# Optimization experiments

Hardware: AMD Instinct MI355X
Metric: run time of the kernel (lower is better)

Reference implementation:

```python
import jax, jax.numpy as jnp
import numpy as np

B, T, D, HS = 8, 2048, 1024, 64  # batch, seq, num_embd, head_size


def setup_inputs() -> dict:
    key = jax.random.key(0)
    kc, kq, kk, kv = jax.random.split(key, 4)
    return {
        "context": jax.random.normal(kc, (B, T, D), dtype=jnp.float32),
        "Wq": jax.random.normal(kq, (D, HS), dtype=jnp.float32) * (D ** -0.5),
        "Wk": jax.random.normal(kk, (D, HS), dtype=jnp.float32) * (D ** -0.5),
        "Wv": jax.random.normal(kv, (D, HS), dtype=jnp.float32) * (D ** -0.5),
    }


def reference(context, Wq, Wk, Wv):
    # context: [B, T, D]; projections: [B, T, HS]
    q = context @ Wq
    k = context @ Wk
    v = context @ Wv
    scale = k.shape[-1] ** -0.5
    # scores: [B, T, T], causal mask, stable softmax (dropout p=0 -> identity)
    wei = jnp.einsum("btd,bsd->bts", q, k) * scale
    t = wei.shape[-1]
    causal = jnp.tril(jnp.ones((t, t), dtype=bool))
    wei = jnp.where(causal, wei, -jnp.inf)
    wei = jax.nn.softmax(wei, axis=-1)
    return jnp.einsum("bts,bsh->bth", wei, v)
```

## Files before the change

kernel.cpp:

```cpp
#include <hip/hip_runtime.h>
#include <math.h>

#define BB 8
#define TT 2048
#define DD 1024
#define HSZ 64

typedef __bf16 bf16_t;
typedef bf16_t bf16x8 __attribute__((ext_vector_type(8)));
typedef bf16_t bf16x4 __attribute__((ext_vector_type(4)));
typedef float f32x4 __attribute__((ext_vector_type(4)));

#define MFMA16(A, B, C) __builtin_amdgcn_mfma_f32_16x16x32_bf16(A, B, C, 0, 0, 0)


__global__ __launch_bounds__(256) void wt_convert(
    const float* __restrict__ Wq, const float* __restrict__ Wk,
    const float* __restrict__ Wv, bf16_t* __restrict__ Wtf)
{
    int id = blockIdx.x * 256 + threadIdx.x;
    int j = id & 7;
    int lane = (id >> 3) & 63;
    int chunk = (id >> 9) & 31;
    int nt = id >> 14;
    int l16 = lane & 15, quad = lane >> 4;
    int k = chunk * 32 + quad * 8 + j;
    int col = nt * 16 + l16;
    int m = col >> 6, ncol = col & 63;
    const float* W = (m == 0) ? Wq : (m == 1) ? Wk : Wv;
    float scl = (m == 0) ? 0.18033688f : 1.0f;
    Wtf[id] = (bf16_t)(W[k * HSZ + ncol] * scl);
}

__global__ __launch_bounds__(256, 3) void qkv_proj(
    const float* __restrict__ ctx, const bf16_t* __restrict__ Wtf,
    bf16_t* __restrict__ Q, bf16_t* __restrict__ Kf, bf16_t* __restrict__ Vf)
{
    __shared__ __align__(16) char smem_raw[16 * 1032 * 2];
    bf16_t (*As)[1032] = (bf16_t (*)[1032])smem_raw;
    f32x4 (*red)[4][64] = (f32x4 (*)[4][64])smem_raw;

    const int tid = threadIdx.x;
    const int w = tid >> 6, lane = tid & 63;
    const int quad = lane >> 4, l16 = lane & 15;
    const size_t row0 = (size_t)blockIdx.x * 16;
    const int k0 = w * 256;

    {
        const float4* csrc = (const float4*)(ctx + row0 * DD);
        #pragma unroll
        for (int i = 0; i < 16; ++i) {
            float4 v = csrc[i * 256 + tid];
            bf16x4 bv;
            bv[0] = (bf16_t)v.x; bv[1] = (bf16_t)v.y;
            bv[2] = (bf16_t)v.z; bv[3] = (bf16_t)v.w;
            *(bf16x4*)&As[i][tid * 4] = bv;
        }
    }
    __syncthreads();

    f32x4 acc[12];
    #pragma unroll
    for (int i = 0; i < 12; ++i) acc[i] = (f32x4){0.f, 0.f, 0.f, 0.f};

    const bf16_t* wbase = Wtf + lane * 8;

    #pragma unroll
    for (int kc = 0; kc < 256; kc += 32) {
        const int chunk = (k0 + kc) >> 5;
        bf16x8 bfr[12];
        #pragma unroll
        for (int nt = 0; nt < 12; ++nt)
            bfr[nt] = *(const bf16x8*)(wbase + ((size_t)nt * 32 + chunk) * 512);
        bf16x8 af = *(const bf16x8*)&As[l16][k0 + kc + quad * 8];
        #pragma unroll
        for (int nt = 0; nt < 12; ++nt)
            acc[nt] = MFMA16(af, bfr[nt], acc[nt]);
    }
    __syncthreads();

    const int bb   = (int)(row0 >> 11);
    const int tloc = (int)(row0 & 2047);
    const int kt   = tloc >> 6;
    const int nn   = (tloc >> 4) & 3;

    #pragma unroll
    for (int r = 0; r < 3; ++r) {
        if (r) __syncthreads();
        #pragma unroll
        for (int i = 0; i < 4; ++i) red[w][i][lane] = acc[r * 4 + i];
        __syncthreads();

        f32x4 s = red[0][w][lane];
        s += red[1][w][lane];
        s += red[2][w][lane];
        s += red[3][w][lane];

        if (r == 0) {
            const int col = w * 16 + l16;
            #pragma unroll
            for (int reg = 0; reg < 4; ++reg)
                Q[(row0 + quad * 4 + reg) * HSZ + col] = (bf16_t)s[reg];
        } else if (r == 1) {
            const int ks = w >> 1;
            const int quadf = (w & 1) * 2 + (l16 >> 3);
            const int jj = l16 & 7;
            const size_t fb = ((((size_t)bb * 32 + kt) * 4 + nn) * 2 + ks) * 512;
            #pragma unroll
            for (int reg = 0; reg < 4; ++reg)
                Kf[fb + (quadf * 16 + quad * 4 + reg) * 8 + jj] = (bf16_t)s[reg];
        } else {
            const int t0 = tloc + quad * 4;
            const int ks = (t0 >> 5) & 1;
            const int quadf = (t0 >> 3) & 3;
            const int j0 = t0 & 7;
            const size_t fb = ((((size_t)bb * 32 + kt) * 2 + ks) * 4 + w) * 512;
            bf16x4 v;
            #pragma unroll
            for (int reg = 0; reg < 4; ++reg) v[reg] = (bf16_t)s[reg];
            *(bf16x4*)(Vf + fb + (quadf * 16 + l16) * 8 + j0) = v;
        }
    }
}

__device__ __forceinline__ void load_kfrags(
    const bf16_t* __restrict__ Kf, size_t bofs, int kt, int lane, bf16x8* kf)
{
    const bf16_t* kbase = Kf + ((bofs + (size_t)kt) * 8) * 512 + lane * 8;
    #pragma unroll
    for (int i = 0; i < 8; ++i)
        kf[i] = *(const bf16x8*)(kbase + i * 512);
}

__global__ __launch_bounds__(64, 3) void attn_kernel(
    const bf16_t* __restrict__ Q, const bf16_t* __restrict__ Kf,
    const bf16_t* __restrict__ Vf,
    float* __restrict__ Opart, float* __restrict__ Lpart)
{
    __shared__ bf16_t Ps[16][76];

    const int lane = threadIdx.x;
    const int quad = lane >> 4, l16 = lane & 15;

    const int z = blockIdx.x;
    const int b = z & 7, c = z >> 3;
    const int j = 127 - (c >> 2);
    const int seg = c & 3;
    const size_t base = (size_t)b * TT * HSZ;
    const size_t bofs = (size_t)b * 32;
    const int ntile = (j >> 2) + 1, jm = j & 3;

    const bf16_t* qp = Q + base + (size_t)(j * 16 + l16) * HSZ + quad * 8;
    bf16x8 qf0 = *(const bf16x8*)qp;
    bf16x8 qf1 = *(const bf16x8*)(qp + 32);

    bf16x8 onesf;
    {
        bf16_t e = (l16 == 0) ? (bf16_t)1.0f : (bf16_t)0.0f;
        #pragma unroll
        for (int i = 0; i < 8; ++i) onesf[i] = e;
    }

    f32x4 o[4];
    #pragma unroll
    for (int dt = 0; dt < 4; ++dt) o[dt] = (f32x4){0.f, 0.f, 0.f, 0.f};
    f32x4 lacc = (f32x4){0.f, 0.f, 0.f, 0.f};

    bf16x8 kA[8], kB[8];

    auto process = [&](int kt, const bf16x8* kf) {
        const bool last = (kt == ntile - 1);
        const int nv = last ? jm + 1 : 4;
        const int ksm = (nv > 2) ? 2 : 1;

        const bf16_t* vbase = Vf + ((bofs + (size_t)kt) * 8) * 512 + lane * 8;
        bf16x8 vf[8];
        #pragma unroll
        for (int i = 0; i < 8; ++i)
            vf[i] = *(const bf16x8*)(vbase + i * 512);

        f32x4 sc[4];
        #pragma unroll
        for (int n = 0; n < 4; ++n) {
            if (n < nv) {
                f32x4 a = (f32x4){0.f, 0.f, 0.f, 0.f};
                a = MFMA16(qf0, kf[2 * n], a);
                a = MFMA16(qf1, kf[2 * n + 1], a);
                sc[n] = a;
            }
        }

        if (last) {
            #pragma unroll
            for (int n = 0; n < 4; ++n) {
                if (n < nv) {
                    #pragma unroll
                    for (int reg = 0; reg < 4; ++reg) {
                        bool masked = (n == jm) && (l16 > quad * 4 + reg);
                        float p = __builtin_amdgcn_exp2f(sc[n][reg]);
                        sc[n][reg] = masked ? 0.f : p;
                    }
                }
            }
        } else {
            #pragma unroll
            for (int n = 0; n < 4; ++n)
                #pragma unroll
                for (int reg = 0; reg < 4; ++reg)
                    sc[n][reg] = __builtin_amdgcn_exp2f(sc[n][reg]);
        }

        #pragma unroll
        for (int n = 0; n < 4; ++n) {
            #pragma unroll
            for (int reg = 0; reg < 4; ++reg) {
                float p = (n < nv) ? sc[n][reg] : 0.f;
                Ps[quad * 4 + reg][n * 16 + l16] = (bf16_t)p;
            }
        }
        bf16x8 pf0 = *(const bf16x8*)&Ps[l16][quad * 8];
        bf16x8 pf1 = *(const bf16x8*)&Ps[l16][32 + quad * 8];

        #pragma unroll
        for (int dt = 0; dt < 4; ++dt) {
            o[dt] = MFMA16(pf0, vf[dt], o[dt]);
            if (ksm == 2) o[dt] = MFMA16(pf1, vf[4 + dt], o[dt]);
        }
        lacc = MFMA16(pf0, onesf, lacc);
        if (ksm == 2) lacc = MFMA16(pf1, onesf, lacc);
    };

    if (seg < ntile) {
        load_kfrags(Kf, bofs, seg, lane, kA);
        for (int kt = seg; kt < ntile; kt += 8) {
            if (kt + 4 < ntile) load_kfrags(Kf, bofs, kt + 4, lane, kB);
            process(kt, kA);
            if (kt + 4 < ntile) {
                if (kt + 8 < ntile) load_kfrags(Kf, bofs, kt + 8, lane, kA);
                process(kt + 4, kB);
            }
        }
    }

    float* op = Opart + (size_t)z * 16 * 64;
    #pragma unroll
    for (int dt = 0; dt < 4; ++dt) {
        #pragma unroll
        for (int reg = 0; reg < 4; ++reg)
            op[(quad * 4 + reg) * 64 + dt * 16 + l16] = o[dt][reg];
    }
    if (l16 == 0) {
        #pragma unroll
        for (int reg = 0; reg < 4; ++reg)
            Lpart[z * 16 + quad * 4 + reg] = lacc[reg];
    }
}

__global__ __launch_bounds__(256) void combine_kernel(
    const float* __restrict__ Opart, const float* __restrict__ Lpart,
    float* __restrict__ O)
{
    int gid = blockIdx.x * 256 + threadIdx.x;
    int col = gid & 63;
    int row = (gid >> 6) & 15;
    int j   = (gid >> 10) & 127;
    int b   = gid >> 17;
    int z0 = ((127 - j) * 4) * 8 + b;
    float l = 0.f, ov = 0.f;
    #pragma unroll
    for (int s = 0; s < 4; ++s) {
        l  += Lpart[(z0 + 8 * s) * 16 + row];
        ov += Opart[((size_t)(z0 + 8 * s) * 16 + row) * 64 + col];
    }
    O[((size_t)b * TT + j * 16 + row) * 64 + col] = ov / l;
}

extern "C" void kernel_launch(void* const* d_in, const int* in_sizes, int n_in,
                              void* d_out, int out_size, void* d_ws, size_t ws_size,
                              hipStream_t stream) {
    const float* ctx = (const float*)d_in[0];
    const float* Wq  = (const float*)d_in[1];
    const float* Wk  = (const float*)d_in[2];
    const float* Wv  = (const float*)d_in[3];
    float* out = (float*)d_out;

    const size_t NQ = (size_t)BB * TT * HSZ;
    bf16_t* Qw  = (bf16_t*)d_ws;
    bf16_t* Kfw = Qw + NQ;
    bf16_t* Vfw = Kfw + NQ;
    bf16_t* Wtf = Vfw + NQ;
    float*  Opart = (float*)(Wtf + 196608);
    float*  Lpart = Opart + (size_t)4096 * 1024;

    wt_convert<<<768, 256, 0, stream>>>(Wq, Wk, Wv, Wtf);
    qkv_proj<<<1024, 256, 0, stream>>>(ctx, Wtf, Qw, Kfw, Vfw);
    attn_kernel<<<4096, 64, 0, stream>>>(Qw, Kfw, Vfw, Opart, Lpart);
    combine_kernel<<<4096, 256, 0, stream>>>(Opart, Lpart, out);
}
```

Before: 128.5 us.

## Fuse split-K combine into attention via 4-wave blocks and LDS reduction

Each attention block now has four wavefronts, one per key-tile segment, instead of launching a separate single-wave block per segment. The partial outputs and row sums are reduced in shared memory, and the normalized result is written straight to the output, so the separate combine kernel and the global Opart/Lpart round trip go away. The MFMA operands are swapped so that P is produced transposed, which allows vectorized bf16x4 stores to LDS. In exchange the waves in a block must all finish before the reduction, so on causal tiles they can wait on each other. The larger block may also lower occupancy.

```diff
diff --git a/kernel.cpp b/kernel.cpp
--- a/kernel.cpp
+++ b/kernel.cpp
@@ -132,20 +132,21 @@
         kf[i] = *(const bf16x8*)(kbase + i * 512);
 }
 
-__global__ __launch_bounds__(64, 3) void attn_kernel(
+__global__ __launch_bounds__(256, 3) void attn_kernel(
     const bf16_t* __restrict__ Q, const bf16_t* __restrict__ Kf,
-    const bf16_t* __restrict__ Vf,
-    float* __restrict__ Opart, float* __restrict__ Lpart)
-{
-    __shared__ bf16_t Ps[16][76];
-
-    const int lane = threadIdx.x;
+    const bf16_t* __restrict__ Vf, float* __restrict__ O)
+{
+    __shared__ bf16_t Ps[4][16][72];
+    __shared__ float Ored[4][16][68];
+    __shared__ float Lred[4][16];
+
+    const int tid = threadIdx.x;
+    const int w = tid >> 6, lane = tid & 63;
     const int quad = lane >> 4, l16 = lane & 15;
 
     const int z = blockIdx.x;
-    const int b = z & 7, c = z >> 3;
-    const int j = 127 - (c >> 2);
-    const int seg = c & 3;
+    const int b = z & 7;
+    const int j = 127 - (z >> 3);
     const size_t base = (size_t)b * TT * HSZ;
     const size_t bofs = (size_t)b * 32;
     const int ntile = (j >> 2) + 1, jm = j & 3;
@@ -154,12 +155,9 @@
     bf16x8 qf0 = *(const bf16x8*)qp;
     bf16x8 qf1 = *(const bf16x8*)(qp + 32);
 
-    bf16x8 onesf;
-    {
-        bf16_t e = (l16 == 0) ? (bf16_t)1.0f : (bf16_t)0.0f;
-        #pragma unroll
-        for (int i = 0; i < 8; ++i) onesf[i] = e;
-    }
+    bf16x8 onesA;
+    #pragma unroll
+    for (int i = 0; i < 8; ++i) onesA[i] = (bf16_t)1.0f;
 
     f32x4 o[4];
     #pragma unroll
@@ -184,8 +182,8 @@
         for (int n = 0; n < 4; ++n) {
             if (n < nv) {
                 f32x4 a = (f32x4){0.f, 0.f, 0.f, 0.f};
-                a = MFMA16(qf0, kf[2 * n], a);
-                a = MFMA16(qf1, kf[2 * n + 1], a);
+                a = MFMA16(kf[2 * n], qf0, a);
+                a = MFMA16(kf[2 * n + 1], qf1, a);
                 sc[n] = a;
             }
         }
@@ -196,7 +194,7 @@
                 if (n < nv) {
                     #pragma unroll
                     for (int reg = 0; reg < 4; ++reg) {
-                        bool masked = (n == jm) && (l16 > quad * 4 + reg);
+                        bool masked = (n == jm) && (quad * 4 + reg > l16);
                         float p = __builtin_amdgcn_exp2f(sc[n][reg]);
                         sc[n][reg] = masked ? 0.f : p;
                     }
@@ -212,27 +210,27 @@
 
         #pragma unroll
         for (int n = 0; n < 4; ++n) {
-            #pragma unroll
-            for (int reg = 0; reg < 4; ++reg) {
-                float p = (n < nv) ? sc[n][reg] : 0.f;
-                Ps[quad * 4 + reg][n * 16 + l16] = (bf16_t)p;
-            }
-        }
-        bf16x8 pf0 = *(const bf16x8*)&Ps[l16][quad * 8];
-        bf16x8 pf1 = *(const bf16x8*)&Ps[l16][32 + quad * 8];
+            bf16x4 pv;
+            #pragma unroll
+            for (int reg = 0; reg < 4; ++reg)
+                pv[reg] = (bf16_t)((n < nv) ? sc[n][reg] : 0.f);
+            *(bf16x4*)&Ps[w][l16][n * 16 + quad * 4] = pv;
+        }
+        bf16x8 pf0 = *(const bf16x8*)&Ps[w][l16][quad * 8];
+        bf16x8 pf1 = *(const bf16x8*)&Ps[w][l16][32 + quad * 8];
 
         #pragma unroll
         for (int dt = 0; dt < 4; ++dt) {
-            o[dt] = MFMA16(pf0, vf[dt], o[dt]);
-            if (ksm == 2) o[dt] = MFMA16(pf1, vf[4 + dt], o[dt]);
-        }
-        lacc = MFMA16(pf0, onesf, lacc);
-        if (ksm == 2) lacc = MFMA16(pf1, onesf, lacc);
+            o[dt] = MFMA16(vf[dt], pf0, o[dt]);
+            if (ksm == 2) o[dt] = MFMA16(vf[4 + dt], pf1, o[dt]);
+        }
+        lacc = MFMA16(onesA, pf0, lacc);
+        if (ksm == 2) lacc = MFMA16(onesA, pf1, lacc);
     };
 
-    if (seg < ntile) {
-        load_kfrags(Kf, bofs, seg, lane, kA);
-        for (int kt = seg; kt < ntile; kt += 8) {
+    if (w < ntile) {
+        load_kfrags(Kf, bofs, w, lane, kA);
+        for (int kt = w; kt < ntile; kt += 8) {
             if (kt + 4 < ntile) load_kfrags(Kf, bofs, kt + 4, lane, kB);
             process(kt, kA);
             if (kt + 4 < ntile) {
@@ -242,37 +240,21 @@
         }
     }
 
-    float* op = Opart + (size_t)z * 16 * 64;
-    #pragma unroll
-    for (int dt = 0; dt < 4; ++dt) {
-        #pragma unroll
-        for (int reg = 0; reg < 4; ++reg)
-            op[(quad * 4 + reg) * 64 + dt * 16 + l16] = o[dt][reg];
-    }
-    if (l16 == 0) {
-        #pragma unroll
-        for (int reg = 0; reg < 4; ++reg)
-            Lpart[z * 16 + quad * 4 + reg] = lacc[reg];
-    }
-}
-
-__global__ __launch_bounds__(256) void combine_kernel(
-    const float* __restrict__ Opart, const float* __restrict__ Lpart,
-    float* __restrict__ O)
-{
-    int gid = blockIdx.x * 256 + threadIdx.x;
-    int col = gid & 63;
-    int row = (gid >> 6) & 15;
-    int j   = (gid >> 10) & 127;
-    int b   = gid >> 17;
-    int z0 = ((127 - j) * 4) * 8 + b;
-    float l = 0.f, ov = 0.f;
-    #pragma unroll
-    for (int s = 0; s < 4; ++s) {
-        l  += Lpart[(z0 + 8 * s) * 16 + row];
-        ov += Opart[((size_t)(z0 + 8 * s) * 16 + row) * 64 + col];
-    }
-    O[((size_t)b * TT + j * 16 + row) * 64 + col] = ov / l;
+    #pragma unroll
+    for (int dt = 0; dt < 4; ++dt)
+        *(f32x4*)&Ored[w][l16][dt * 16 + quad * 4] = o[dt];
+    if (quad == 0) Lred[w][l16] = lacc[0];
+    __syncthreads();
+
+    const int query = tid >> 4, d4 = tid & 15;
+    float l = Lred[0][query] + Lred[1][query] + Lred[2][query] + Lred[3][query];
+    f32x4 s = *(const f32x4*)&Ored[0][query][d4 * 4];
+    s += *(const f32x4*)&Ored[1][query][d4 * 4];
+    s += *(const f32x4*)&Ored[2][query][d4 * 4];
+    s += *(const f32x4*)&Ored[3][query][d4 * 4];
+    const float linv = 1.f / l;
+    float4 outv = make_float4(s[0] * linv, s[1] * linv, s[2] * linv, s[3] * linv);
+    *(float4*)(O + base + (size_t)(j * 16 + query) * HSZ + d4 * 4) = outv;
 }
 
 extern "C" void kernel_launch(void* const* d_in, const int* in_sizes, int n_in,
@@ -289,11 +271,8 @@
     bf16_t* Kfw = Qw + NQ;
     bf16_t* Vfw = Kfw + NQ;
     bf16_t* Wtf = Vfw + NQ;
-    float*  Opart = (float*)(Wtf + 196608);
-    float*  Lpart = Opart + (size_t)4096 * 1024;
 
     wt_convert<<<768, 256, 0, stream>>>(Wq, Wk, Wv, Wtf);
     qkv_proj<<<1024, 256, 0, stream>>>(ctx, Wtf, Qw, Kfw, Vfw);
-    attn_kernel<<<4096, 64, 0, stream>>>(Qw, Kfw, Vfw, Opart, Lpart);
-    combine_kernel<<<4096, 256, 0, stream>>>(Opart, Lpart, out);
-}
+    attn_kernel<<<1024, 256, 0, stream>>>(Qw, Kfw, Vfw, out);
+}
```

Result: faster. 122.8 us (-4.5%).
